# Kernel tuning notes

Hardware: AMD Instinct MI355X
Metric: run time of the kernel (lower is better)

The kernel has to match this reference:

```python
import jax, jax.numpy as jnp
import numpy as np

B, S, EMBED, HEADS = 2, 2048, 1024, 16
HEAD = EMBED // HEADS


def setup_inputs() -> dict:
    key = jax.random.key(0)
    ks = jax.random.split(key, 8)
    inp = {
        "values": jax.random.normal(ks[0], (B, S, EMBED), jnp.float32),
        "keys": jax.random.normal(ks[1], (B, S, EMBED), jnp.float32),
        "queries": jax.random.normal(ks[2], (B, S, EMBED), jnp.float32),
        # causal mask, broadcast over batch and heads; masked_fill where mask==0
        "mask": jnp.tril(jnp.ones((S, S), jnp.bool_))[None, None, :, :],
        # torch nn.Linear weights: y = x @ W.T (+ b)
        "Wv": jax.random.normal(ks[3], (HEAD, HEAD), jnp.float32) / np.sqrt(HEAD),
        "Wk": jax.random.normal(ks[4], (HEAD, HEAD), jnp.float32) / np.sqrt(HEAD),
        "Wq": jax.random.normal(ks[5], (HEAD, HEAD), jnp.float32) / np.sqrt(HEAD),
        "Wo": jax.random.normal(ks[6], (EMBED, EMBED), jnp.float32) / np.sqrt(EMBED),
        "bo": jax.random.normal(ks[7], (EMBED,), jnp.float32) * 0.01,
    }
    return inp


def reference(values, keys, queries, mask, Wv, Wk, Wq, Wo, bo):
    N, Lq = queries.shape[0], queries.shape[1]
    Lk = keys.shape[1]
    # split heads: [B, L, H, D]
    v = values.reshape(N, -1, HEADS, HEAD) @ Wv.T
    k = keys.reshape(N, Lk, HEADS, HEAD) @ Wk.T
    q = queries.reshape(N, Lq, HEADS, HEAD) @ Wq.T
    # scores [B, H, Lq, Lk]
    energy = jnp.einsum('bqhd,bkhd->bhqk', q, k)
    energy = jnp.where(mask, energy, jnp.float32(-1e20))
    attn = jax.nn.softmax(energy / np.sqrt(HEAD), axis=-1)
    out = jnp.einsum('bhqk,bkhd->bqhd', attn, v).reshape(N, Lq, EMBED)
    return out @ Wo.T + bo
```

## Files before the change

kernel.cpp:

```cpp
#include <hip/hip_runtime.h>
#include <hip/hip_bf16.h>
#include <math.h>

constexpr int Bc = 2;
constexpr int Sc = 2048;
constexpr int E  = 1024;
constexpr int Hn = 16;
constexpr int Dh = 64;

typedef short bf16x8 __attribute__((ext_vector_type(8)));
typedef float f32x4  __attribute__((ext_vector_type(4)));

#define MFMA16(a, b, c) __builtin_amdgcn_mfma_f32_16x16x32_bf16((a), (b), (c), 0, 0, 0)

constexpr float QSCALE = 0.125f * 1.4426950408889634f;
constexpr float FIXED_M2 = 18.0f;

__device__ inline bf16x8 load8(const __hip_bfloat16* p) {
    return *reinterpret_cast<const bf16x8*>(p);
}

__device__ inline unsigned short f2b(float x) {
    __hip_bfloat16 h = __float2bfloat16(x);
    unsigned short u;
    __builtin_memcpy(&u, &h, 2);
    return u;
}

__device__ inline ushort4 pack4(float a, float b, float c, float d) {
    __hip_bfloat162 lo = __float22bfloat162_rn(make_float2(a, b));
    __hip_bfloat162 hi = __float22bfloat162_rn(make_float2(c, d));
    ushort4 u;
    __builtin_memcpy(&u.x, &lo, 4);
    __builtin_memcpy(&u.z, &hi, 4);
    return u;
}

__device__ inline bf16x8 cvt8(const float* p) {
    float4 a = *reinterpret_cast<const float4*>(p);
    float4 b = *reinterpret_cast<const float4*>(p + 4);
    ushort4 lo = pack4(a.x, a.y, a.z, a.w);
    ushort4 hi = pack4(b.x, b.y, b.z, b.w);
    bf16x8 r;
    __builtin_memcpy(&r, &lo, 8);
    __builtin_memcpy(reinterpret_cast<char*>(&r) + 8, &hi, 8);
    return r;
}

__device__ inline float fast_exp2(float x) {
#if __has_builtin(__builtin_amdgcn_exp2f)
    return __builtin_amdgcn_exp2f(x);
#else
    return exp2f(x);
#endif
}


__global__ __launch_bounds__(256) void cvt_w(
    const float* __restrict__ Wo, const float* __restrict__ Wq,
    const float* __restrict__ Wk, const float* __restrict__ Wv,
    __hip_bfloat16* __restrict__ Wf, __hip_bfloat16* __restrict__ Wf3) {
    const int i = blockIdx.x * 256 + threadIdx.x;
    if (i < 131072) {
        const int l16 = i & 15, quad = (i >> 4) & 3;
        const int kk = (i >> 6) & 31, ct = i >> 11;
        bf16x8 v = cvt8(Wo + (size_t)(ct * 16 + l16) * E + kk * 32 + quad * 8);
        *reinterpret_cast<bf16x8*>(Wf + (size_t)i * 8) = v;
    } else {
        const int idx = i - 131072;
        const int m = idx >> 9, r = idx & 511;
        const int lane = r & 63, nh = r >> 6;
        const int nt = nh >> 1, half = nh & 1;
        const int quad = lane >> 4, l16 = lane & 15;
        const float* Wm = (m == 0) ? Wq : (m == 1) ? Wk : Wv;
        bf16x8 v = cvt8(Wm + (nt * 16 + l16) * 64 + half * 32 + quad * 8);
        *reinterpret_cast<bf16x8*>(Wf3 + (size_t)idx * 8) = v;
    }
}

__global__ __launch_bounds__(256) void qkv_proj(
    const float* __restrict__ vals,
    const float* __restrict__ keys,
    const float* __restrict__ quer,
    const __hip_bfloat16* __restrict__ Wf3,
    __hip_bfloat16* __restrict__ Qf,
    __hip_bfloat16* __restrict__ Kf,
    __hip_bfloat16* __restrict__ Vf)
{
    __shared__ __align__(16) __hip_bfloat16 X[3][64 * 72];

    const int bid = blockIdx.x;
    const int st  = bid & 31;
    const int h   = (bid >> 5) & 15;
    const int b   = bid >> 9;
    const int sbase = st * 64;
    const int tid = threadIdx.x;

    const float* srcs[3] = { quer, keys, vals };
#pragma unroll
    for (int m = 0; m < 3; ++m) {
        for (int i = tid; i < 1024; i += 256) {
            const int r = i >> 4, c = i & 15;
            float4 f = *reinterpret_cast<const float4*>(
                srcs[m] + (size_t)(b * Sc + sbase + r) * E + h * 64 + c * 4);
            *reinterpret_cast<ushort4*>(&X[m][r * 72 + c * 4]) =
                pack4(f.x, f.y, f.z, f.w);
        }
    }
    __syncthreads();

    const int lane = tid & 63, w = tid >> 6;
    const int quad = lane >> 4, l16 = lane & 15;
    const int bh = b * Hn + h;
    const size_t bhoff = (size_t)bh * 131072;

#pragma unroll
    for (int m = 0; m < 2; ++m) {
        bf16x8 xb0 = load8(&X[m][(w * 16 + l16) * 72 + quad * 8]);
        bf16x8 xb1 = load8(&X[m][(w * 16 + l16) * 72 + quad * 8 + 32]);
#pragma unroll
        for (int ntd = 0; ntd < 4; ++ntd) {
            bf16x8 wa0 = load8(Wf3 + ((size_t)(m * 8 + ntd * 2 + 0) * 64 + lane) * 8);
            bf16x8 wa1 = load8(Wf3 + ((size_t)(m * 8 + ntd * 2 + 1) * 64 + lane) * 8);
            f32x4 acc = (f32x4){0.f, 0.f, 0.f, 0.f};
            acc = MFMA16(wa0, xb0, acc);
            acc = MFMA16(wa1, xb1, acc);
            const int half   = ntd >> 1;
            const int quad_f = (ntd & 1) * 2 + (quad >> 1);
            const int j0     = (quad & 1) * 4;
            if (m == 0) {
                const int t = st * 4 + w;
                *reinterpret_cast<ushort4*>(
                    Qf + bhoff + ((size_t)(t * 2 + half) * 64 + quad_f * 16 + l16) * 8 + j0) =
                    pack4(acc[0] * QSCALE, acc[1] * QSCALE, acc[2] * QSCALE, acc[3] * QSCALE);
            } else {
                *reinterpret_cast<ushort4*>(
                    Kf + bhoff + (((size_t)(st * 4 + w) * 2 + half) * 64 + quad_f * 16 + l16) * 8 + j0) =
                    pack4(acc[0], acc[1], acc[2], acc[3]);
            }
        }
    }

    {
        bf16x8 xa0 = load8(&X[2][(w * 16 + l16) * 72 + quad * 8]);
        bf16x8 xa1 = load8(&X[2][(w * 16 + l16) * 72 + quad * 8 + 32]);
        const int half   = w >> 1;
        const int quad_f = (w & 1) * 2 + (quad >> 1);
        const int j0     = (quad & 1) * 4;
#pragma unroll
        for (int nt = 0; nt < 4; ++nt) {
            bf16x8 wb0 = load8(Wf3 + ((size_t)(16 + nt * 2 + 0) * 64 + lane) * 8);
            bf16x8 wb1 = load8(Wf3 + ((size_t)(16 + nt * 2 + 1) * 64 + lane) * 8);
            f32x4 acc = (f32x4){0.f, 0.f, 0.f, 0.f};
            acc = MFMA16(xa0, wb0, acc);
            acc = MFMA16(xa1, wb1, acc);
            *reinterpret_cast<ushort4*>(
                Vf + bhoff + (((size_t)(st * 4 + nt) * 2 + half) * 64 + quad_f * 16 + l16) * 8 + j0) =
                pack4(acc[0], acc[1], acc[2], acc[3]);
        }
    }
}

__global__ __launch_bounds__(128) void flash_attn(
    const __hip_bfloat16* __restrict__ Qf,
    const __hip_bfloat16* __restrict__ Kf,
    const __hip_bfloat16* __restrict__ Vf,
    __hip_bfloat16* __restrict__ Af)
{
    __shared__ __align__(16) __hip_bfloat16 P[2][16 * 72];
    __shared__ __align__(16) float OB[2][16 * 68];
    __shared__ float LB[2][16];

    const int bid = blockIdx.x;
    const int bh = bid & 31;
    const int j  = bid >> 5;
    const int h  = bh & 15;
    const int b  = bh >> 4;
    const int tid = threadIdx.x, lane = tid & 63, w = tid >> 6;
    const int quad = lane >> 4, l16 = lane & 15;
    const int hf = w;

    const __hip_bfloat16* Qp = Qf + (size_t)bh * 131072;
    const __hip_bfloat16* Kp = Kf + (size_t)bh * 131072;
    const __hip_bfloat16* Vp = Vf + (size_t)bh * 131072;

#pragma unroll
    for (int side = 0; side < 2; ++side) {
        const int t  = side ? j : (127 - j);
        const int nk = (t >> 2) + 1;
        const int r0 = t * 16;

        const bf16x8 qf0 = load8(Qp + ((size_t)(t * 2 + 0) * 64 + lane) * 8);
        const bf16x8 qf1 = load8(Qp + ((size_t)(t * 2 + 1) * 64 + lane) * 8);

        f32x4 oa[4];
#pragma unroll
        for (int nt = 0; nt < 4; ++nt) oa[nt] = (f32x4){0.f, 0.f, 0.f, 0.f};
        float ls = 0.f;

        if (hf < nk) {
            bf16x8 ka[4], kb[4];
#pragma unroll
            for (int nt = 0; nt < 4; ++nt) {
                const size_t o = (((size_t)hf * 4 + nt) * 2) * 64 * 8;
                ka[nt] = load8(Kp + o + lane * 8);
                kb[nt] = load8(Kp + o + 512 + lane * 8);
            }
            for (int kt = hf; kt < nk; kt += 2) {
                bf16x8 va[4], vb[4];
#pragma unroll
                for (int nt = 0; nt < 4; ++nt) {
                    const size_t o = (((size_t)kt * 4 + nt) * 2) * 64 * 8;
                    va[nt] = load8(Vp + o + lane * 8);
                    vb[nt] = load8(Vp + o + 512 + lane * 8);
                }
                const int nkt = (kt + 2 < nk) ? kt + 2 : kt;
                bf16x8 na[4], nb[4];
#pragma unroll
                for (int nt = 0; nt < 4; ++nt) {
                    const size_t o = (((size_t)nkt * 4 + nt) * 2) * 64 * 8;
                    na[nt] = load8(Kp + o + lane * 8);
                    nb[nt] = load8(Kp + o + 512 + lane * 8);
                }
                const int kbase = kt * 64;
                f32x4 sc[4];
#pragma unroll
                for (int ntk = 0; ntk < 4; ++ntk) {
                    f32x4 z = (f32x4){0.f, 0.f, 0.f, 0.f};
                    z = MFMA16(ka[ntk], qf0, z);
                    z = MFMA16(kb[ntk], qf1, z);
                    sc[ntk] = z;
                }
                if (kt == nk - 1) {
                    const int qrow = r0 + l16;
#pragma unroll
                    for (int ntk = 0; ntk < 4; ++ntk) {
#pragma unroll
                        for (int r = 0; r < 4; ++r)
                            if (kbase + ntk * 16 + quad * 4 + r > qrow)
                                sc[ntk][r] = -1e30f;
                    }
                }
#pragma unroll
                for (int ntk = 0; ntk < 4; ++ntk) {
                    const float p0 = fast_exp2(sc[ntk][0] - FIXED_M2);
                    const float p1 = fast_exp2(sc[ntk][1] - FIXED_M2);
                    const float p2 = fast_exp2(sc[ntk][2] - FIXED_M2);
                    const float p3 = fast_exp2(sc[ntk][3] - FIXED_M2);
                    ls += (p0 + p1) + (p2 + p3);
                    *reinterpret_cast<ushort4*>(
                        &P[w][l16 * 72 + ntk * 16 + quad * 4]) = pack4(p0, p1, p2, p3);
                }
                bf16x8 pf0 = load8(&P[w][l16 * 72 + quad * 8]);
                bf16x8 pf1 = load8(&P[w][l16 * 72 + quad * 8 + 32]);
#pragma unroll
                for (int nt = 0; nt < 4; ++nt) {
                    oa[nt] = MFMA16(va[nt], pf0, oa[nt]);
                    oa[nt] = MFMA16(vb[nt], pf1, oa[nt]);
                }
#pragma unroll
                for (int nt = 0; nt < 4; ++nt) { ka[nt] = na[nt]; kb[nt] = nb[nt]; }
            }
        }
        ls += __shfl_xor(ls, 16);
        ls += __shfl_xor(ls, 32);

        if (hf == 1) {
#pragma unroll
            for (int nt = 0; nt < 4; ++nt)
                *reinterpret_cast<float4*>(&OB[side][l16 * 68 + nt * 16 + quad * 4]) =
                    (float4){ oa[nt][0], oa[nt][1], oa[nt][2], oa[nt][3] };
            if (quad == 0) LB[side][l16] = ls;
        }
        __syncthreads();
        if (hf == 0) {
            const float inv = 1.0f / (ls + LB[side][l16]);
            const int rt = b * 128 + t;
#pragma unroll
            for (int nt = 0; nt < 4; ++nt) {
                float4 ob = *reinterpret_cast<float4*>(&OB[side][l16 * 68 + nt * 16 + quad * 4]);
                const int kk     = h * 2 + (nt >> 1);
                const int quad_f = (nt & 1) * 2 + (quad >> 1);
                const int j0     = (quad & 1) * 4;
                *reinterpret_cast<ushort4*>(
                    Af + (((size_t)rt * 32 + kk) * 64 + quad_f * 16 + l16) * 8 + j0) =
                    pack4((oa[nt][0] + ob.x) * inv, (oa[nt][1] + ob.y) * inv,
                          (oa[nt][2] + ob.z) * inv, (oa[nt][3] + ob.w) * inv);
            }
        }
    }
}

__global__ __launch_bounds__(256) void out_proj(
    const __hip_bfloat16* __restrict__ Af,
    const __hip_bfloat16* __restrict__ Wf,
    const float* __restrict__ bo,
    float* __restrict__ out)
{
    const int bid = blockIdx.x;
    const int cb = bid & 15;
    const int rb = bid >> 4;
    const int tid = threadIdx.x, lane = tid & 63, w = tid >> 6;
    const int quad = lane >> 4, l16 = lane & 15;
    const int rt0 = rb * 8 + w;
    const int cbase = cb * 64;

    const __hip_bfloat16* pa0 = Af + ((size_t)rt0 * 32) * 512 + lane * 8;
    const __hip_bfloat16* pa1 = pa0 + 4 * 32 * 512;
    const __hip_bfloat16* pw  = Wf + ((size_t)cb * 4 * 32) * 512 + lane * 8;

    f32x4 acc[2][4];
#pragma unroll
    for (int u = 0; u < 2; ++u)
#pragma unroll
        for (int nt = 0; nt < 4; ++nt) acc[u][nt] = (f32x4){0.f, 0.f, 0.f, 0.f};

    bf16x8 af0 = load8(pa0), af1 = load8(pa1);
    bf16x8 bf[4];
#pragma unroll
    for (int nt = 0; nt < 4; ++nt) bf[nt] = load8(pw + (size_t)nt * 32 * 512);

    for (int kk = 0; kk < 32; ++kk) {
        const size_t ko = (size_t)((kk < 31) ? kk + 1 : kk) * 512;
        bf16x8 naf0 = load8(pa0 + ko), naf1 = load8(pa1 + ko);
        bf16x8 nbf[4];
#pragma unroll
        for (int nt = 0; nt < 4; ++nt) nbf[nt] = load8(pw + (size_t)nt * 32 * 512 + ko);
#pragma unroll
        for (int nt = 0; nt < 4; ++nt) {
            acc[0][nt] = MFMA16(af0, bf[nt], acc[0][nt]);
            acc[1][nt] = MFMA16(af1, bf[nt], acc[1][nt]);
        }
        af0 = naf0; af1 = naf1;
#pragma unroll
        for (int nt = 0; nt < 4; ++nt) bf[nt] = nbf[nt];
    }
#pragma unroll
    for (int nt = 0; nt < 4; ++nt) {
        const float bv = bo[cbase + nt * 16 + l16];
#pragma unroll
        for (int u = 0; u < 2; ++u)
#pragma unroll
            for (int r = 0; r < 4; ++r) {
                const int row = (rt0 + u * 4) * 16 + quad * 4 + r;
                out[(size_t)row * E + cbase + nt * 16 + l16] = acc[u][nt][r] + bv;
            }
    }
}

extern "C" void kernel_launch(void* const* d_in, const int* in_sizes, int n_in,
                              void* d_out, int out_size, void* d_ws, size_t ws_size,
                              hipStream_t stream) {
    const float* vals = (const float*)d_in[0];
    const float* keys = (const float*)d_in[1];
    const float* quer = (const float*)d_in[2];
    const float* Wv = (const float*)d_in[4];
    const float* Wk = (const float*)d_in[5];
    const float* Wq = (const float*)d_in[6];
    const float* Wo = (const float*)d_in[7];
    const float* bo = (const float*)d_in[8];
    float* out = (float*)d_out;

    __hip_bfloat16* ws = (__hip_bfloat16*)d_ws;
    constexpr size_t NTOK = (size_t)Bc * Hn * Sc * Dh;
    __hip_bfloat16* Qw  = ws;
    __hip_bfloat16* Kw  = ws + NTOK;
    __hip_bfloat16* Vw  = ws + 2 * NTOK;
    __hip_bfloat16* Aw  = ws + 3 * NTOK;
    __hip_bfloat16* Wof = ws + 4 * NTOK;
    __hip_bfloat16* Wf3 = Wof + (size_t)E * E;

    hipLaunchKernelGGL(cvt_w, dim3(518), dim3(256), 0, stream, Wo, Wq, Wk, Wv, Wof, Wf3);
    hipLaunchKernelGGL(qkv_proj, dim3(Bc * Hn * (Sc / 64)), dim3(256), 0, stream,
                       vals, keys, quer, Wf3, Qw, Kw, Vw);
    hipLaunchKernelGGL(flash_attn, dim3(64 * 32), dim3(128), 0, stream,
                       Qw, Kw, Vw, Aw);
    hipLaunchKernelGGL(out_proj, dim3(32 * 16), dim3(256), 0, stream,
                       Aw, Wof, bo, out);
}
```

Baseline: 182.0 us.

## Pack two query-tile pairs per attention block, MFMA row sums, deeper out_proj prefetch

Several independent changes land together. The attention kernel now runs 256 threads per block and covers two query-tile pairs per block, halving the grid. Softmax row sums are computed with an MFMA against a ones vector instead of scalar adds and cross-lane shuffles. The out_proj K loop prefetches two steps ahead, and qkv_proj loads 8 floats per thread through a cvt8 helper. The costs are extra registers and shared memory, more MFMA issues per tile, and a dependency on cvt8 being defined in the hidden part of the file.

```diff
diff --git a/kernel.cpp b/kernel.cpp
--- a/kernel.cpp
+++ b/kernel.cpp
@@ -99,12 +99,10 @@
     const float* srcs[3] = { quer, keys, vals };
 #pragma unroll
     for (int m = 0; m < 3; ++m) {
-        for (int i = tid; i < 1024; i += 256) {
-            const int r = i >> 4, c = i & 15;
-            float4 f = *reinterpret_cast<const float4*>(
-                srcs[m] + (size_t)(b * Sc + sbase + r) * E + h * 64 + c * 4);
-            *reinterpret_cast<ushort4*>(&X[m][r * 72 + c * 4]) =
-                pack4(f.x, f.y, f.z, f.w);
+        for (int i = tid; i < 512; i += 256) {
+            const int r = i >> 3, c = i & 7;
+            bf16x8 v = cvt8(srcs[m] + (size_t)(b * Sc + sbase + r) * E + h * 64 + c * 8);
+            *reinterpret_cast<bf16x8*>(&X[m][r * 72 + c * 8]) = v;
         }
     }
     __syncthreads();
@@ -161,28 +159,34 @@
     }
 }
 
-__global__ __launch_bounds__(128) void flash_attn(
+__global__ __launch_bounds__(256) void flash_attn(
     const __hip_bfloat16* __restrict__ Qf,
     const __hip_bfloat16* __restrict__ Kf,
     const __hip_bfloat16* __restrict__ Vf,
     __hip_bfloat16* __restrict__ Af)
 {
-    __shared__ __align__(16) __hip_bfloat16 P[2][16 * 72];
-    __shared__ __align__(16) float OB[2][16 * 68];
-    __shared__ float LB[2][16];
+    __shared__ __align__(16) __hip_bfloat16 P[4][16 * 72];
+    __shared__ __align__(16) float OB[4][16 * 68];
+    __shared__ float LB[4][16];
 
     const int bid = blockIdx.x;
     const int bh = bid & 31;
-    const int j  = bid >> 5;
+    const int ip = bid >> 5;
     const int h  = bh & 15;
     const int b  = bh >> 4;
     const int tid = threadIdx.x, lane = tid & 63, w = tid >> 6;
     const int quad = lane >> 4, l16 = lane & 15;
-    const int hf = w;
+    const int p  = w >> 1;
+    const int hf = w & 1;
+    const int j  = ip * 2 + p;
 
     const __hip_bfloat16* Qp = Qf + (size_t)bh * 131072;
     const __hip_bfloat16* Kp = Kf + (size_t)bh * 131072;
     const __hip_bfloat16* Vp = Vf + (size_t)bh * 131072;
+
+    bf16x8 onesf;
+#pragma unroll
+    for (int q = 0; q < 8; ++q) onesf[q] = (short)0x3F80;
 
 #pragma unroll
     for (int side = 0; side < 2; ++side) {
@@ -196,7 +200,7 @@
         f32x4 oa[4];
 #pragma unroll
         for (int nt = 0; nt < 4; ++nt) oa[nt] = (f32x4){0.f, 0.f, 0.f, 0.f};
-        float ls = 0.f;
+        f32x4 lsacc = (f32x4){0.f, 0.f, 0.f, 0.f};
 
         if (hf < nk) {
             bf16x8 ka[4], kb[4];
@@ -247,7 +251,6 @@
                     const float p1 = fast_exp2(sc[ntk][1] - FIXED_M2);
                     const float p2 = fast_exp2(sc[ntk][2] - FIXED_M2);
                     const float p3 = fast_exp2(sc[ntk][3] - FIXED_M2);
-                    ls += (p0 + p1) + (p2 + p3);
                     *reinterpret_cast<ushort4*>(
                         &P[w][l16 * 72 + ntk * 16 + quad * 4]) = pack4(p0, p1, p2, p3);
                 }
@@ -258,27 +261,29 @@
                     oa[nt] = MFMA16(va[nt], pf0, oa[nt]);
                     oa[nt] = MFMA16(vb[nt], pf1, oa[nt]);
                 }
+                lsacc = MFMA16(onesf, pf0, lsacc);
+                lsacc = MFMA16(onesf, pf1, lsacc);
 #pragma unroll
                 for (int nt = 0; nt < 4; ++nt) { ka[nt] = na[nt]; kb[nt] = nb[nt]; }
             }
         }
-        ls += __shfl_xor(ls, 16);
-        ls += __shfl_xor(ls, 32);
-
+        const float ls = lsacc[0];
+
+        const int slot = p * 2 + side;
         if (hf == 1) {
 #pragma unroll
             for (int nt = 0; nt < 4; ++nt)
-                *reinterpret_cast<float4*>(&OB[side][l16 * 68 + nt * 16 + quad * 4]) =
+                *reinterpret_cast<float4*>(&OB[slot][l16 * 68 + nt * 16 + quad * 4]) =
                     (float4){ oa[nt][0], oa[nt][1], oa[nt][2], oa[nt][3] };
-            if (quad == 0) LB[side][l16] = ls;
+            if (quad == 0) LB[slot][l16] = ls;
         }
         __syncthreads();
         if (hf == 0) {
-            const float inv = 1.0f / (ls + LB[side][l16]);
+            const float inv = 1.0f / (ls + LB[slot][l16]);
             const int rt = b * 128 + t;
 #pragma unroll
             for (int nt = 0; nt < 4; ++nt) {
-                float4 ob = *reinterpret_cast<float4*>(&OB[side][l16 * 68 + nt * 16 + quad * 4]);
+                float4 ob = *reinterpret_cast<float4*>(&OB[slot][l16 * 68 + nt * 16 + quad * 4]);
                 const int kk     = h * 2 + (nt >> 1);
                 const int quad_f = (nt & 1) * 2 + (quad >> 1);
                 const int j0     = (quad & 1) * 4;
@@ -315,25 +320,34 @@
 #pragma unroll
         for (int nt = 0; nt < 4; ++nt) acc[u][nt] = (f32x4){0.f, 0.f, 0.f, 0.f};
 
-    bf16x8 af0 = load8(pa0), af1 = load8(pa1);
-    bf16x8 bf[4];
-#pragma unroll
-    for (int nt = 0; nt < 4; ++nt) bf[nt] = load8(pw + (size_t)nt * 32 * 512);
-
-    for (int kk = 0; kk < 32; ++kk) {
-        const size_t ko = (size_t)((kk < 31) ? kk + 1 : kk) * 512;
-        bf16x8 naf0 = load8(pa0 + ko), naf1 = load8(pa1 + ko);
-        bf16x8 nbf[4];
-#pragma unroll
-        for (int nt = 0; nt < 4; ++nt) nbf[nt] = load8(pw + (size_t)nt * 32 * 512 + ko);
-#pragma unroll
-        for (int nt = 0; nt < 4; ++nt) {
-            acc[0][nt] = MFMA16(af0, bf[nt], acc[0][nt]);
-            acc[1][nt] = MFMA16(af1, bf[nt], acc[1][nt]);
-        }
-        af0 = naf0; af1 = naf1;
-#pragma unroll
-        for (int nt = 0; nt < 4; ++nt) bf[nt] = nbf[nt];
+    bf16x8 af0[2], af1[2], bf[4][2];
+#pragma unroll
+    for (int s = 0; s < 2; ++s) {
+        const size_t ko = (size_t)s * 512;
+        af0[s] = load8(pa0 + ko);
+        af1[s] = load8(pa1 + ko);
+#pragma unroll
+        for (int nt = 0; nt < 4; ++nt) bf[nt][s] = load8(pw + (size_t)nt * 32 * 512 + ko);
+    }
+
+    for (int kk = 0; kk < 32; kk += 2) {
+#pragma unroll
+        for (int s = 0; s < 2; ++s) {
+            const int kn = kk + 2 + s;
+            const size_t ko = (size_t)((kn < 32) ? kn : kk + s) * 512;
+            bf16x8 naf0 = load8(pa0 + ko), naf1 = load8(pa1 + ko);
+            bf16x8 nbf[4];
+#pragma unroll
+            for (int nt = 0; nt < 4; ++nt) nbf[nt] = load8(pw + (size_t)nt * 32 * 512 + ko);
+#pragma unroll
+            for (int nt = 0; nt < 4; ++nt) {
+                acc[0][nt] = MFMA16(af0[s], bf[nt][s], acc[0][nt]);
+                acc[1][nt] = MFMA16(af1[s], bf[nt][s], acc[1][nt]);
+            }
+            af0[s] = naf0; af1[s] = naf1;
+#pragma unroll
+            for (int nt = 0; nt < 4; ++nt) bf[nt][s] = nbf[nt];
+        }
     }
 #pragma unroll
     for (int nt = 0; nt < 4; ++nt) {
@@ -373,7 +387,7 @@
     hipLaunchKernelGGL(cvt_w, dim3(518), dim3(256), 0, stream, Wo, Wq, Wk, Wv, Wof, Wf3);
     hipLaunchKernelGGL(qkv_proj, dim3(Bc * Hn * (Sc / 64)), dim3(256), 0, stream,
                        vals, keys, quer, Wf3, Qw, Kw, Vw);
-    hipLaunchKernelGGL(flash_attn, dim3(64 * 32), dim3(128), 0, stream,
+    hipLaunchKernelGGL(flash_attn, dim3(32 * 32), dim3(256), 0, stream,
                        Qw, Kw, Vw, Aw);
     hipLaunchKernelGGL(out_proj, dim3(32 * 16), dim3(256), 0, stream,
                        Aw, Wof, bo, out);
```

Result: faster. 176.3 us (-3.1%).
